# Kernel tuning notes

Hardware: AMD Instinct MI355X
Metric: run time of the kernel (lower is better)

The kernel has to match this reference:

```python
import jax, jax.numpy as jnp
import numpy as np

N_PARENT = 50000   # parent voxels
C_IN = 256
C_OUT = 256
FANOUT = 8         # children per parent (kernel 2, stride 2 generative conv)
N_TGT = 200000     # number of ground-truth-occupied child indices


def setup_inputs() -> dict:
    key = jax.random.key(0)
    k_fea, k_wup, k_wcls, k_idx = jax.random.split(key, 4)
    fea = jax.random.normal(k_fea, (N_PARENT, C_IN), dtype=jnp.float32)
    W_up = jax.random.normal(k_wup, (FANOUT, C_IN, C_OUT), dtype=jnp.float32) * (1.0 / np.sqrt(C_IN))
    b_up = jnp.zeros((C_OUT,), dtype=jnp.float32)
    W_cls = jax.random.normal(k_wcls, (C_OUT, 1), dtype=jnp.float32) * (1.0 / np.sqrt(C_OUT))
    b_cls = jnp.zeros((1,), dtype=jnp.float32)
    # kernel_map in-indices into the upsampled coordinate set (GT-occupied children)
    target_idx = jax.random.randint(k_idx, (N_TGT,), 0, N_PARENT * FANOUT, dtype=jnp.int64)
    return {"fea": fea, "W_up": W_up, "b_up": b_up, "W_cls": W_cls,
            "b_cls": b_cls, "target_idx": target_idx}


def reference(fea, W_up, b_up, W_cls, b_cls, target_idx):
    # upsample_block: generative transposed sparse conv. Every parent voxel emits
    # FANOUT children, each via its own [C_IN, C_OUT] kernel slice.
    # [N, C_IN] x [K, C_IN, C_OUT] -> [N, K, C_OUT] -> [N*K, C_OUT]
    fea_up = jnp.einsum('nc,kcd->nkd', fea, W_up).reshape(-1, W_up.shape[2]) + b_up
    # classify_block: 1-channel existence logit
    exist = fea_up @ W_cls + b_cls                      # [N*K, 1]
    # keep = exist > 0 (computed under no_grad in torch)
    keep = jax.lax.stop_gradient(exist[:, 0]) > 0       # [N*K] bool
    # kernel_map target scatter: target[curr_in] = 1
    n_up = fea_up.shape[0]
    target = jnp.zeros((n_up,), dtype=jnp.bool_).at[target_idx].set(True)
    keep = keep | target                                # training: keep |= target
    # MinkowskiPruning(fea, keep): jit-compatible masking instead of compaction
    fea_pruned = jnp.where(keep[:, None], fea_up, jnp.zeros((), fea_up.dtype))
    return fea_pruned, exist, target
```

## Files before the change

kernel.cpp:

```cpp
#include <hip/hip_runtime.h>
#include <hip/hip_bf16.h>

#define N_PARENT 50000
#define C_IN     256
#define C_OUT    256
#define FANOUT   8
#define N_TGT    200000
#define N_UP     (N_PARENT * FANOUT)
#define NCOL     (FANOUT * C_OUT)
#define NSTRIP   391
#define NROWS    (NSTRIP * 128)

#define OFF_A    0u
#define OFF_B    (NSTRIP * 65536u)
#define OFF_V    (OFF_B + 16u * 65536u)
#define OFF_EB   (OFF_V + 8192u)
#define OFF_KEEP (OFF_EB + 256u)

typedef __attribute__((ext_vector_type(8))) short short8;
typedef __attribute__((ext_vector_type(4))) float floatx4;

static __device__ __forceinline__ unsigned short f2bf(float f) {
    return __builtin_bit_cast(unsigned short, __float2bfloat16(f));
}

static __device__ __forceinline__ void gload_lds16(const void* gsrc, void* ldsdst) {
    __builtin_amdgcn_global_load_lds(
        (const __attribute__((address_space(1))) unsigned int*)gsrc,
        (__attribute__((address_space(3))) unsigned int*)ldsdst, 16, 0, 0);
}

__global__ __launch_bounds__(256) void prep_kernel(
        const float* __restrict__ W_up, const float* __restrict__ b_up,
        const float* __restrict__ W_cls, const float* __restrict__ b_cls,
        unsigned char* __restrict__ ws, float* __restrict__ out2) {
    __shared__ float sm[4];
    const int bid = blockIdx.x;
    const int k = bid >> 8, c = bid & 255;
    const int d = threadIdx.x;

    if (d < 49) {
        const int i4 = bid * 49 + d;
        if (i4 < N_UP / 4)
            *(floatx4*)&out2[i4 * 4] = (floatx4){0.f, 0.f, 0.f, 0.f};
    }

    const float w = W_up[((k * 256 + c) * 256) + d];
    const int bn = (k << 1) | (d >> 7);
    const int jr = d & 127;
    const int ks = c >> 6;
    const int cc = (c >> 3) & 7;
    const int e  = c & 7;
    const unsigned off = OFF_B + (unsigned)bn * 65536u + (unsigned)ks * 16384u
                       + (unsigned)jr * 128u + (unsigned)((cc ^ (jr & 7)) << 4)
                       + (unsigned)(e << 1);
    *(unsigned short*)(ws + off) = f2bf(w);

    float p = w * W_cls[d];
    #pragma unroll
    for (int m = 1; m < 64; m <<= 1) p += __shfl_xor(p, m);
    if ((d & 63) == 0) sm[d >> 6] = p;
    __syncthreads();
    if (d == 0)
        ((float*)(ws + OFF_V))[k * 256 + c] = sm[0] + sm[1] + sm[2] + sm[3];

    if (bid == 0) {
        __syncthreads();
        float q = b_up[d] * W_cls[d];
        #pragma unroll
        for (int m = 1; m < 64; m <<= 1) q += __shfl_xor(q, m);
        if ((d & 63) == 0) sm[d >> 6] = q;
        __syncthreads();
        if (d == 0)
            *((float*)(ws + OFF_EB)) = sm[0] + sm[1] + sm[2] + sm[3] + b_cls[0];
    }
}

__global__ __launch_bounds__(256) void scatter_kernel(
        const int* __restrict__ idx, float* __restrict__ out2) {
    int i = blockIdx.x * 256 + threadIdx.x;
    if (i < N_TGT) out2[idx[i]] = 1.0f;
}

__global__ __launch_bounds__(256) void convert_kernel(
        const float* __restrict__ fea, const float* __restrict__ target,
        float* __restrict__ out1, unsigned char* __restrict__ ws) {
    const float* V = (const float*)(ws + OFF_V);
    const float eb = *(const float*)(ws + OFF_EB);

    const int rowid = blockIdx.x * 4 + (threadIdx.x >> 6);
    const int lane  = threadIdx.x & 63;
    const bool valid = rowid < N_PARENT;

    floatx4 f = (floatx4){0.f, 0.f, 0.f, 0.f};
    if (valid)
        f = __builtin_nontemporal_load(
                (const floatx4*)&fea[(size_t)rowid * C_IN + lane * 4]);

    float ex[8];
    #pragma unroll
    for (int k = 0; k < 8; ++k) {
        const float4 v = *(const float4*)&V[k * 256 + lane * 4];
        ex[k] = f[0] * v.x + f[1] * v.y + f[2] * v.z + f[3] * v.w;
    }

    const unsigned long long pk =
          (unsigned long long)f2bf(f[0])
        | ((unsigned long long)f2bf(f[1]) << 16)
        | ((unsigned long long)f2bf(f[2]) << 32)
        | ((unsigned long long)f2bf(f[3]) << 48);
    const int strip = rowid >> 7, r = rowid & 127;
    const int ks = lane >> 4, cc = (lane >> 1) & 7, half = lane & 1;
    const unsigned off = OFF_A + (unsigned)strip * 65536u + (unsigned)ks * 16384u
                       + (unsigned)r * 128u + (unsigned)((cc ^ (r & 7)) << 4)
                       + (unsigned)(half * 8);
    *(unsigned long long*)(ws + off) = pk;

    #pragma unroll
    for (int m = 8; m < 64; m <<= 1)
        #pragma unroll
        for (int k = 0; k < 8; ++k) ex[k] += __shfl_xor(ex[k], m);

    const int ksel = lane >> 3;
    float v = ex[0];
    #pragma unroll
    for (int k = 1; k < 8; ++k) v = (ksel == k) ? ex[k] : v;
    #pragma unroll
    for (int m = 1; m < 8; m <<= 1) v += __shfl_xor(v, m);
    v += eb;

    if ((lane & 7) == 0 && valid) {
        const size_t o = (size_t)rowid * FANOUT + ksel;
        out1[o] = v;
        ws[OFF_KEEP + o] = ((v > 0.0f) || (target[o] != 0.0f)) ? 1 : 0;
    }
}

__global__ __launch_bounds__(256) void gemm_kernel(
        const float* __restrict__ b_up, const unsigned char* __restrict__ ws,
        float* __restrict__ out0) {
    __shared__ unsigned short As[8192];
    __shared__ unsigned short Bs[8192];
    __shared__ unsigned char keeps[128];

    const int bid = blockIdx.x;
    const int g = bid & 7, u = bid >> 3;
    const int t = u >> 4, bn = u & 15;
    const int bm = g + 8 * t;
    if (bm >= NSTRIP) return;

    const unsigned char* Abase = ws + OFF_A + (size_t)bm * 65536u;
    const unsigned char* Bbase = ws + OFF_B + (size_t)bn * 65536u;

    const int tid  = threadIdx.x;
    const int lane = tid & 63;
    const int wid  = tid >> 6;
    const int wr = wid >> 1, wc = wid & 1;
    const int llo = lane & 15, lhi = lane >> 4;

    if (tid < 128) {
        const int n = bm * 128 + tid;
        keeps[tid] = (n < N_PARENT) ? ws[OFF_KEEP + (size_t)n * FANOUT + (bn >> 1)] : 0;
    }

    floatx4 acc[4][4];
    #pragma unroll
    for (int a = 0; a < 4; ++a)
        #pragma unroll
        for (int b = 0; b < 4; ++b) acc[a][b] = (floatx4){0.f, 0.f, 0.f, 0.f};

    for (int ks = 0; ks < 4; ++ks) {
        #pragma unroll
        for (int it = 0; it < 4; ++it)
            gload_lds16(Abase + ks * 16384 + it * 4096 + tid * 16,
                        (char*)As + it * 4096 + tid * 16);
        #pragma unroll
        for (int it = 0; it < 4; ++it)
            gload_lds16(Bbase + ks * 16384 + it * 4096 + tid * 16,
                        (char*)Bs + it * 4096 + tid * 16);
        __syncthreads();

        #pragma unroll
        for (int h = 0; h < 2; ++h) {
            short8 af[4], bf[4];
            #pragma unroll
            for (int fm = 0; fm < 4; ++fm) {
                const int row = wr * 64 + fm * 16 + llo;
                const int ch = (h * 4 + lhi) ^ (row & 7);
                af[fm] = *(const short8*)((const char*)As + row * 128 + ch * 16);
            }
            #pragma unroll
            for (int fn = 0; fn < 4; ++fn) {
                const int row = wc * 64 + fn * 16 + llo;
                const int ch = (h * 4 + lhi) ^ (row & 7);
                bf[fn] = *(const short8*)((const char*)Bs + row * 128 + ch * 16);
            }
            #pragma unroll
            for (int fm = 0; fm < 4; ++fm)
                #pragma unroll
                for (int fn = 0; fn < 4; ++fn)
                    acc[fm][fn] = __builtin_amdgcn_mfma_f32_16x16x32_bf16(
                        bf[fn], af[fm], acc[fm][fn], 0, 0, 0);
        }
        if (ks < 3) __syncthreads();
    }

    const int j0 = bn * 128;
    #pragma unroll
    for (int fm = 0; fm < 4; ++fm) {
        const int row = wr * 64 + fm * 16 + llo;
        const int m = bm * 128 + row;
        if (m >= N_PARENT) continue;
        const bool kp = keeps[row] != 0;
        #pragma unroll
        for (int fn = 0; fn < 4; ++fn) {
            const int j = j0 + wc * 64 + fn * 16 + lhi * 4;
            const float4 bv = *(const float4*)&b_up[j & 255];
            const floatx4 a = acc[fm][fn];
            floatx4 o;
            o[0] = kp ? a[0] + bv.x : 0.0f;
            o[1] = kp ? a[1] + bv.y : 0.0f;
            o[2] = kp ? a[2] + bv.z : 0.0f;
            o[3] = kp ? a[3] + bv.w : 0.0f;
            __builtin_nontemporal_store(o, (floatx4*)&out0[(size_t)m * NCOL + j]);
        }
    }
}

extern "C" void kernel_launch(void* const* d_in, const int* in_sizes, int n_in,
                              void* d_out, int out_size, void* d_ws, size_t ws_size,
                              hipStream_t stream) {
    const float* fea   = (const float*)d_in[0];
    const float* W_up  = (const float*)d_in[1];
    const float* b_up  = (const float*)d_in[2];
    const float* W_cls = (const float*)d_in[3];
    const float* b_cls = (const float*)d_in[4];
    const int*   tidx  = (const int*)d_in[5];

    float* out0 = (float*)d_out;
    float* out1 = out0 + (size_t)N_UP * C_OUT;
    float* out2 = out1 + N_UP;
    unsigned char* ws = (unsigned char*)d_ws;

    prep_kernel<<<2048, 256, 0, stream>>>(W_up, b_up, W_cls, b_cls, ws, out2);
    scatter_kernel<<<(N_TGT + 255) / 256, 256, 0, stream>>>(tidx, out2);
    convert_kernel<<<NROWS / 4, 256, 0, stream>>>(fea, out2, out1, ws);
    gemm_kernel<<<392 * 16, 256, 0, stream>>>(b_up, ws, out0);
}
```

Measured before the change: 149.1 us.

## Double-buffer LDS tiles in GEMM with K-chunks of 32

The bf16 A and B workspace layouts are reorganized into 32-wide K chunks with a 4-way XOR swizzle, written by the prep and feature kernels. The GEMM kernel now keeps two LDS buffers and prefetches the next chunk while running MFMAs on the current one, with one barrier per step. The aim is to overlap global-to-LDS loads with compute instead of stalling at each barrier. It also adds a launch_bounds occupancy hint of 4. The cost is twice as many barrier steps, each covering less MFMA work, and extra register pressure from the hint.

```diff
diff --git a/kernel.cpp b/kernel.cpp
--- a/kernel.cpp
+++ b/kernel.cpp
@@ -48,11 +48,11 @@
     const float w = W_up[((k * 256 + c) * 256) + d];
     const int bn = (k << 1) | (d >> 7);
     const int jr = d & 127;
-    const int ks = c >> 6;
-    const int cc = (c >> 3) & 7;
+    const int t  = c >> 5;
+    const int ch = (c >> 3) & 3;
     const int e  = c & 7;
-    const unsigned off = OFF_B + (unsigned)bn * 65536u + (unsigned)ks * 16384u
-                       + (unsigned)jr * 128u + (unsigned)((cc ^ (jr & 7)) << 4)
+    const unsigned off = OFF_B + (unsigned)bn * 65536u + (unsigned)t * 8192u
+                       + (unsigned)jr * 64u + (unsigned)((ch ^ (jr & 3)) << 4)
                        + (unsigned)(e << 1);
     *(unsigned short*)(ws + off) = f2bf(w);
 
@@ -110,9 +110,9 @@
         | ((unsigned long long)f2bf(f[2]) << 32)
         | ((unsigned long long)f2bf(f[3]) << 48);
     const int strip = rowid >> 7, r = rowid & 127;
-    const int ks = lane >> 4, cc = (lane >> 1) & 7, half = lane & 1;
-    const unsigned off = OFF_A + (unsigned)strip * 65536u + (unsigned)ks * 16384u
-                       + (unsigned)r * 128u + (unsigned)((cc ^ (r & 7)) << 4)
+    const int t = lane >> 3, ch = (lane >> 1) & 3, half = lane & 1;
+    const unsigned off = OFF_A + (unsigned)strip * 65536u + (unsigned)t * 8192u
+                       + (unsigned)r * 64u + (unsigned)((ch ^ (r & 3)) << 4)
                        + (unsigned)(half * 8);
     *(unsigned long long*)(ws + off) = pk;
 
@@ -136,17 +136,17 @@
     }
 }
 
-__global__ __launch_bounds__(256) void gemm_kernel(
+__global__ __launch_bounds__(256, 4) void gemm_kernel(
         const float* __restrict__ b_up, const unsigned char* __restrict__ ws,
         float* __restrict__ out0) {
-    __shared__ unsigned short As[8192];
-    __shared__ unsigned short Bs[8192];
+    __shared__ unsigned short As[2][4096];
+    __shared__ unsigned short Bs[2][4096];
     __shared__ unsigned char keeps[128];
 
     const int bid = blockIdx.x;
     const int g = bid & 7, u = bid >> 3;
-    const int t = u >> 4, bn = u & 15;
-    const int bm = g + 8 * t;
+    const int tt = u >> 4, bn = u & 15;
+    const int bm = g + 8 * tt;
     if (bm >= NSTRIP) return;
 
     const unsigned char* Abase = ws + OFF_A + (size_t)bm * 65536u;
@@ -169,40 +169,44 @@
         #pragma unroll
         for (int b = 0; b < 4; ++b) acc[a][b] = (floatx4){0.f, 0.f, 0.f, 0.f};
 
-    for (int ks = 0; ks < 4; ++ks) {
-        #pragma unroll
-        for (int it = 0; it < 4; ++it)
-            gload_lds16(Abase + ks * 16384 + it * 4096 + tid * 16,
-                        (char*)As + it * 4096 + tid * 16);
-        #pragma unroll
-        for (int it = 0; it < 4; ++it)
-            gload_lds16(Bbase + ks * 16384 + it * 4096 + tid * 16,
-                        (char*)Bs + it * 4096 + tid * 16);
-        __syncthreads();
-
-        #pragma unroll
-        for (int h = 0; h < 2; ++h) {
-            short8 af[4], bf[4];
+    gload_lds16(Abase + tid * 16,        (char*)As[0] + tid * 16);
+    gload_lds16(Abase + 4096 + tid * 16, (char*)As[0] + 4096 + tid * 16);
+    gload_lds16(Bbase + tid * 16,        (char*)Bs[0] + tid * 16);
+    gload_lds16(Bbase + 4096 + tid * 16, (char*)Bs[0] + 4096 + tid * 16);
+    __syncthreads();
+
+    #pragma unroll
+    for (int t = 0; t < 8; ++t) {
+        const int cur = t & 1;
+        if (t < 7) {
+            const unsigned o = (unsigned)(t + 1) * 8192u;
+            gload_lds16(Abase + o + tid * 16,        (char*)As[cur ^ 1] + tid * 16);
+            gload_lds16(Abase + o + 4096 + tid * 16, (char*)As[cur ^ 1] + 4096 + tid * 16);
+            gload_lds16(Bbase + o + tid * 16,        (char*)Bs[cur ^ 1] + tid * 16);
+            gload_lds16(Bbase + o + 4096 + tid * 16, (char*)Bs[cur ^ 1] + 4096 + tid * 16);
+        }
+
+        short8 af[4], bf[4];
+        #pragma unroll
+        for (int fm = 0; fm < 4; ++fm) {
+            const int row = wr * 64 + fm * 16 + llo;
+            const int ch = lhi ^ (row & 3);
+            af[fm] = *(const short8*)((const char*)As[cur] + row * 64 + ch * 16);
+        }
+        #pragma unroll
+        for (int fn = 0; fn < 4; ++fn) {
+            const int row = wc * 64 + fn * 16 + llo;
+            const int ch = lhi ^ (row & 3);
+            bf[fn] = *(const short8*)((const char*)Bs[cur] + row * 64 + ch * 16);
+        }
+        #pragma unroll
+        for (int fm = 0; fm < 4; ++fm)
             #pragma unroll
-            for (int fm = 0; fm < 4; ++fm) {
-                const int row = wr * 64 + fm * 16 + llo;
-                const int ch = (h * 4 + lhi) ^ (row & 7);
-                af[fm] = *(const short8*)((const char*)As + row * 128 + ch * 16);
-            }
-            #pragma unroll
-            for (int fn = 0; fn < 4; ++fn) {
-                const int row = wc * 64 + fn * 16 + llo;
-                const int ch = (h * 4 + lhi) ^ (row & 7);
-                bf[fn] = *(const short8*)((const char*)Bs + row * 128 + ch * 16);
-            }
-            #pragma unroll
-            for (int fm = 0; fm < 4; ++fm)
-                #pragma unroll
-                for (int fn = 0; fn < 4; ++fn)
-                    acc[fm][fn] = __builtin_amdgcn_mfma_f32_16x16x32_bf16(
-                        bf[fn], af[fm], acc[fm][fn], 0, 0, 0);
-        }
-        if (ks < 3) __syncthreads();
+            for (int fn = 0; fn < 4; ++fn)
+                acc[fm][fn] = __builtin_amdgcn_mfma_f32_16x16x32_bf16(
+                    bf[fn], af[fm], acc[fm][fn], 0, 0, 0);
+
+        if (t < 7) __syncthreads();
     }
 
     const int j0 = bn * 128;
```

After: 151.1 us. Within noise of the previous version (+1.3%).
